# Performance work log

Hardware: AMD Instinct MI355X
Metric: run time of the kernel (lower is better)

The kernel has to match this reference:

```python
import jax, jax.numpy as jnp
import numpy as np

V, E, H, B, S = 32000, 1024, 1024, 64, 128


def setup_inputs() -> dict:
    key = jax.random.key(0)
    ks = jax.random.split(key, 16)
    s = 0.02
    return {
        "input_seq": jax.random.randint(ks[0], (B, 1), 0, V),
        "hidden": jax.random.normal(ks[1], (1, B, H), jnp.float32),
        "cell": jax.random.normal(ks[2], (1, B, H), jnp.float32),
        "encoder_outputs": jax.random.normal(ks[3], (B, S, H), jnp.float32),
        "emb": jax.random.normal(ks[4], (V, E), jnp.float32) * s,
        "Wa_w": jax.random.normal(ks[5], (H, H), jnp.float32) * s,
        "Wa_b": jnp.zeros((H,), jnp.float32),
        "Ua_w": jax.random.normal(ks[6], (H, H), jnp.float32) * s,
        "Ua_b": jnp.zeros((H,), jnp.float32),
        "Va_w": jax.random.normal(ks[7], (1, H), jnp.float32) * s,
        "Va_b": jnp.zeros((1,), jnp.float32),
        "W_ih": jax.random.normal(ks[8], (4 * H, E + H), jnp.float32) * s,
        "W_hh": jax.random.normal(ks[9], (4 * H, H), jnp.float32) * s,
        "b_ih": jnp.zeros((4 * H,), jnp.float32),
        "b_hh": jnp.zeros((4 * H,), jnp.float32),
        "out_w": jax.random.normal(ks[10], (V, H), jnp.float32) * s,
        "out_b": jnp.zeros((V,), jnp.float32),
    }


def reference(input_seq, hidden, cell, encoder_outputs, emb, Wa_w, Wa_b, Ua_w, Ua_b,
              Va_w, Va_b, W_ih, W_hh, b_ih, b_hh, out_w, out_b):
    # embedding lookup (dropout p=0 -> identity): [B,1,E]
    embedded = emb[input_seq]
    # query = last layer hidden: [B,1,H]
    query = hidden[-1][:, None, :]
    # Bahdanau additive attention
    q_proj = query @ Wa_w.T + Wa_b                       # [B,1,H]
    k_proj = encoder_outputs @ Ua_w.T + Ua_b             # [B,S,H]
    scores = jnp.tanh(q_proj + k_proj) @ Va_w.T + Va_b   # [B,S,1]
    scores = scores[..., 0][:, None, :]                  # [B,1,S]
    weights = jax.nn.softmax(scores, axis=-1)            # [B,1,S]
    context = jnp.einsum('bqs,bsh->bqh', weights, encoder_outputs)  # [B,1,H]
    # LSTM single step on concat(embedded, context)
    x = jnp.concatenate([embedded, context], axis=2)[:, 0, :]  # [B,E+H]
    h0, c0 = hidden[0], cell[0]
    gates = x @ W_ih.T + b_ih + h0 @ W_hh.T + b_hh       # [B,4H]
    i, f, g, o = jnp.split(gates, 4, axis=-1)
    c1 = jax.nn.sigmoid(f) * c0 + jax.nn.sigmoid(i) * jnp.tanh(g)
    h1 = jax.nn.sigmoid(o) * jnp.tanh(c1)
    output = h1[:, None, :]                              # [B,1,H]
    logits = output @ out_w.T + out_b                    # [B,1,V]
    return logits, h1[None], c1[None], weights
```

## Files before the change

kernel.cpp:

```cpp
#include <hip/hip_runtime.h>
#include <hip/hip_bf16.h>

using short8 = __attribute__((ext_vector_type(8))) short;
using f32x4  = __attribute__((ext_vector_type(4))) float;

__device__ inline unsigned pk2(float lo, float hi) {
    __hip_bfloat162 h = __float22bfloat162_rn(float2{lo, hi});
    return *reinterpret_cast<unsigned*>(&h);
}
__device__ inline short8 cvt8(float4 a, float4 b) {
    union { unsigned u[4]; short8 s; } r;
    r.u[0] = pk2(a.x, a.y); r.u[1] = pk2(a.z, a.w);
    r.u[2] = pk2(b.x, b.y); r.u[3] = pk2(b.z, b.w);
    return r.s;
}
__device__ inline float ftanh(float x) {
    float e = __expf(2.f * x);
    return 1.f - 2.f / (e + 1.f);
}
__device__ inline void gload16(const void* g, void* lds) {
    __builtin_amdgcn_global_load_lds(
        (const __attribute__((address_space(1))) unsigned int*)g,
        (__attribute__((address_space(3))) unsigned int*)lds, 16, 0, 0);
}
__device__ inline short f2b(float f) {
    unsigned u = __float_as_uint(f);
    return (short)((u + 0x7FFFu + ((u >> 16) & 1u)) >> 16);
}

__global__ void k_init(const int* __restrict__ idx, const float* __restrict__ emb,
                       const float* __restrict__ h0, short* __restrict__ xcat_bf,
                       float4* __restrict__ wsz) {
    int i = blockIdx.x * blockDim.x + threadIdx.x;
    if (i < 18432) {
        float4 z = {0.f, 0.f, 0.f, 0.f};
        wsz[i] = z;
    } else if (i < 34816) {
        int j = i - 18432;
        int b = j >> 8, g = j & 255;
        if (g < 128) {
            const float* p = emb + (size_t)idx[b] * 1024 + g * 8;
            *(short8*)&xcat_bf[b * 3072 + g * 8] =
                cvt8(*(const float4*)p, *(const float4*)(p + 4));
        } else {
            const float* p = h0 + (size_t)b * 1024 + (g - 128) * 8;
            *(short8*)&xcat_bf[b * 3072 + 2048 + (g - 128) * 8] =
                cvt8(*(const float4*)p, *(const float4*)(p + 4));
        }
    }
}

__global__ void k_cvt_swz(const float* __restrict__ enc, const float* __restrict__ Ua,
                          short* __restrict__ dst) {
    int i = blockIdx.x * blockDim.x + threadIdx.x;
    if (i >= 9216 * 128) return;
    int row = i >> 7, gi = i & 127;
    int seg = gi >> 3, g = gi & 7;
    const float* src = (row < 8192) ? enc + ((size_t)row << 10)
                                    : Ua + ((size_t)(row - 8192) << 10);
    const float* p = src + (seg << 6) + ((g ^ (row & 7)) << 3);
    float4 v0 = *(const float4*)p;
    float4 v1 = *(const float4*)(p + 4);
    *(short8*)&dst[(size_t)i << 3] = cvt8(v0, v1);
}

__global__ __launch_bounds__(512) void k_attn2(
    const short* __restrict__ Abf, const short* __restrict__ Bbf,
    const float* __restrict__ Uab, const float* __restrict__ Wab,
    const float* __restrict__ qp, const float* __restrict__ Va,
    float* __restrict__ scores) {
    __shared__ short As[256 * 64];
    __shared__ short Bs[128 * 64];
    const int t = threadIdx.x;
    const int l = t & 63, w = t >> 6;
    const int wm = w >> 1, wn = w & 1;
    const int lr = l & 15, lg = l >> 4;
    const int n0 = blockIdx.x * 128;
    const int r0 = blockIdx.y * 256;

    f32x4 acc[4][4];
#pragma unroll
    for (int i = 0; i < 4; ++i)
#pragma unroll
        for (int j = 0; j < 4; ++j) { f32x4 z = {0.f, 0.f, 0.f, 0.f}; acc[i][j] = z; }

    for (int seg = 0; seg < 16; ++seg) {
#pragma unroll
        for (int i = 0; i < 4; ++i) {
            int base = i * 512 + w * 64;
            int s = base + l;
            gload16(Abf + (((size_t)r0 + (s >> 3)) << 10) + (seg << 6) + ((s & 7) << 3),
                    (void*)&As[base * 8]);
            if (i < 2)
                gload16(Bbf + (((size_t)8192 + n0 + (s >> 3)) << 10) + (seg << 6) + ((s & 7) << 3),
                        (void*)&Bs[base * 8]);
        }
        __syncthreads();
#pragma unroll
        for (int kh = 0; kh < 2; ++kh) {
            short8 a[4], b[4];
#pragma unroll
            for (int i = 0; i < 4; ++i) {
                int ra = wm * 64 + i * 16 + lr;
                a[i] = *(const short8*)&As[ra * 64 + (((kh * 4 + lg) ^ (ra & 7)) << 3)];
                int rb = wn * 64 + i * 16 + lr;
                b[i] = *(const short8*)&Bs[rb * 64 + (((kh * 4 + lg) ^ (rb & 7)) << 3)];
            }
#pragma unroll
            for (int i = 0; i < 4; ++i)
#pragma unroll
                for (int j = 0; j < 4; ++j)
                    acc[i][j] = __builtin_amdgcn_mfma_f32_16x16x32_bf16(a[i], b[j], acc[i][j], 0, 0, 0);
        }
        __syncthreads();
    }

    float va[4], ub[4];
#pragma unroll
    for (int j = 0; j < 4; ++j) {
        int h = n0 + wn * 64 + j * 16 + lr;
        va[j] = Va[h];
        ub[j] = Uab[h] + Wab[h];
    }
#pragma unroll
    for (int i = 0; i < 4; ++i)
#pragma unroll
        for (int r = 0; r < 4; ++r) {
            int row = r0 + wm * 64 + i * 16 + lg * 4 + r;
            const float* qpb = qp + (size_t)(row >> 7) * 1024;
            float s = 0.f;
#pragma unroll
            for (int j = 0; j < 4; ++j) {
                int h = n0 + wn * 64 + j * 16 + lr;
                s += va[j] * ftanh(acc[i][j][r] + qpb[h] + ub[j]);
            }
            s += __shfl_xor(s, 1);
            s += __shfl_xor(s, 2);
            s += __shfl_xor(s, 4);
            s += __shfl_xor(s, 8);
            if (lr == 0) atomicAdd(scores + row, s);
        }
}

__global__ __launch_bounds__(256) void k_sgemm(
    const float* __restrict__ A, int lda,
    const float* __restrict__ B0, int ldb0,
    float* __restrict__ C, int ldc, int Kblk) {
    __shared__ short As[64 * 64];
    __shared__ short Bs[64 * 64];
    const int t = threadIdx.x;
    const int l = t & 63, w = t >> 6;
    const int wm = w >> 1, wn = w & 1;
    const int lr = l & 15, lg = l >> 4;
    const int n0 = blockIdx.x * 64;
    const int ky = blockIdx.y;

    const float* Ab = A + (size_t)ky * Kblk;
    const float* Bb = B0 + (size_t)ky * Kblk;

    f32x4 acc[2][2];
#pragma unroll
    for (int i = 0; i < 2; ++i)
#pragma unroll
        for (int j = 0; j < 2; ++j) { f32x4 z = {0.f, 0.f, 0.f, 0.f}; acc[i][j] = z; }

    for (int kt = 0; kt < Kblk; kt += 64) {
#pragma unroll
        for (int i = 0; i < 2; ++i) {
            int s = t + 256 * i, row = s >> 3, ch = s & 7;
            const float* p = Ab + (size_t)row * lda + kt + ch * 8;
            *(short8*)&As[row * 64 + ((ch ^ (row & 7)) << 3)] =
                cvt8(*(const float4*)p, *(const float4*)(p + 4));
            const float* q = Bb + (size_t)(n0 + row) * ldb0 + kt + ch * 8;
            *(short8*)&Bs[row * 64 + ((ch ^ (row & 7)) << 3)] =
                cvt8(*(const float4*)q, *(const float4*)(q + 4));
        }
        __syncthreads();
#pragma unroll
        for (int kh = 0; kh < 2; ++kh) {
            short8 a[2], b[2];
#pragma unroll
            for (int i = 0; i < 2; ++i) {
                int ra = wm * 32 + i * 16 + lr;
                a[i] = *(const short8*)&As[ra * 64 + (((kh * 4 + lg) ^ (ra & 7)) << 3)];
                int rb = wn * 32 + i * 16 + lr;
                b[i] = *(const short8*)&Bs[rb * 64 + (((kh * 4 + lg) ^ (rb & 7)) << 3)];
            }
#pragma unroll
            for (int i = 0; i < 2; ++i)
#pragma unroll
                for (int j = 0; j < 2; ++j)
                    acc[i][j] = __builtin_amdgcn_mfma_f32_16x16x32_bf16(a[i], b[j], acc[i][j], 0, 0, 0);
        }
        __syncthreads();
    }

#pragma unroll
    for (int i = 0; i < 2; ++i)
#pragma unroll
        for (int j = 0; j < 2; ++j)
#pragma unroll
            for (int r = 0; r < 4; ++r) {
                int R = wm * 32 + i * 16 + lg * 4 + r;
                int c = n0 + wn * 32 + j * 16 + lr;
                atomicAdd(&C[(size_t)R * ldc + c], acc[i][j][r]);
            }
}

__global__ __launch_bounds__(64) void k_gates_s(
    const short* __restrict__ Abf, const float* __restrict__ Wih,
    const float* __restrict__ Whh, float* __restrict__ gp) {
    const int l = threadIdx.x;
    const int lr = l & 15, lg = l >> 4;
    const int n0 = blockIdx.x * 16;
    const int ky = blockIdx.y;
    const float* Bb = (ky == 0) ? Wih : (ky == 1) ? Wih + 1024 : Whh;
    const int ldb = (ky < 2) ? 2048 : 1024;

    f32x4 acc[4];
#pragma unroll
    for (int i = 0; i < 4; ++i) { f32x4 z = {0.f, 0.f, 0.f, 0.f}; acc[i] = z; }

    const short* ap = Abf + lr * 3072 + ky * 1024 + lg * 8;
    const float* bp = Bb + (size_t)(n0 + lr) * ldb + lg * 8;

#pragma unroll 4
    for (int k0 = 0; k0 < 1024; k0 += 32) {
        float4 b0 = *(const float4*)(bp + k0);
        float4 b1 = *(const float4*)(bp + k0 + 4);
        short8 bf = cvt8(b0, b1);
        short8 a0 = *(const short8*)(ap + k0);
        short8 a1 = *(const short8*)(ap + k0 + 16 * 3072);
        short8 a2 = *(const short8*)(ap + k0 + 32 * 3072);
        short8 a3 = *(const short8*)(ap + k0 + 48 * 3072);
        acc[0] = __builtin_amdgcn_mfma_f32_16x16x32_bf16(a0, bf, acc[0], 0, 0, 0);
        acc[1] = __builtin_amdgcn_mfma_f32_16x16x32_bf16(a1, bf, acc[1], 0, 0, 0);
        acc[2] = __builtin_amdgcn_mfma_f32_16x16x32_bf16(a2, bf, acc[2], 0, 0, 0);
        acc[3] = __builtin_amdgcn_mfma_f32_16x16x32_bf16(a3, bf, acc[3], 0, 0, 0);
    }

    float* Cp = gp + (size_t)ky * 262144;
#pragma unroll
    for (int i = 0; i < 4; ++i)
#pragma unroll
        for (int r = 0; r < 4; ++r)
            Cp[(size_t)(i * 16 + lg * 4 + r) * 4096 + n0 + lr] = acc[i][r];
}

__global__ __launch_bounds__(64) void k_logits_s(
    const short* __restrict__ Abf, const float* __restrict__ B,
    const float* __restrict__ bias, float* __restrict__ C) {
    const int l = threadIdx.x;
    const int lr = l & 15, lg = l >> 4;
    const int n0 = blockIdx.x * 16;

    f32x4 acc[4];
#pragma unroll
    for (int i = 0; i < 4; ++i) { f32x4 z = {0.f, 0.f, 0.f, 0.f}; acc[i] = z; }

    const short* ap = Abf + lr * 1024 + lg * 8;
    const float* bp = B + (size_t)(n0 + lr) * 1024 + lg * 8;

#pragma unroll 4
    for (int k0 = 0; k0 < 1024; k0 += 32) {
        float4 b0 = *(const float4*)(bp + k0);
        float4 b1 = *(const float4*)(bp + k0 + 4);
        short8 bf = cvt8(b0, b1);
        short8 a0 = *(const short8*)(ap + k0);
        short8 a1 = *(const short8*)(ap + k0 + 16 * 1024);
        short8 a2 = *(const short8*)(ap + k0 + 32 * 1024);
        short8 a3 = *(const short8*)(ap + k0 + 48 * 1024);
        acc[0] = __builtin_amdgcn_mfma_f32_16x16x32_bf16(a0, bf, acc[0], 0, 0, 0);
        acc[1] = __builtin_amdgcn_mfma_f32_16x16x32_bf16(a1, bf, acc[1], 0, 0, 0);
        acc[2] = __builtin_amdgcn_mfma_f32_16x16x32_bf16(a2, bf, acc[2], 0, 0, 0);
        acc[3] = __builtin_amdgcn_mfma_f32_16x16x32_bf16(a3, bf, acc[3], 0, 0, 0);
    }

    float bv = bias[n0 + lr];
#pragma unroll
    for (int i = 0; i < 4; ++i)
#pragma unroll
        for (int r = 0; r < 4; ++r)
            C[(size_t)(i * 16 + lg * 4 + r) * 32000 + n0 + lr] = acc[i][r] + bv;
}

__global__ __launch_bounds__(256) void k_smctx(
    const float* __restrict__ scores, const float* __restrict__ enc,
    float* __restrict__ wout, short* __restrict__ xcat_bf) {
    int b = blockIdx.x;
    int t = threadIdx.x;
    __shared__ float buf[128];
    __shared__ float wsb[128];
    if (t < 128) buf[t] = scores[b * 128 + t];
    __syncthreads();
    if (t < 64) buf[t] = fmaxf(buf[t], buf[t + 64]);
    __syncthreads();
    if (t < 32) buf[t] = fmaxf(buf[t], buf[t + 32]);
    __syncthreads();
    float m;
    {
        float v = buf[t & 31];
        for (int off = 16; off > 0; off >>= 1)
            v = fmaxf(v, __shfl_xor(v, off, 32));
        m = v;
    }
    __syncthreads();
    if (t < 128) wsb[t] = __expf(scores[b * 128 + t] - m);
    __syncthreads();
    if (t < 64) buf[t] = wsb[t] + wsb[t + 64];
    __syncthreads();
    if (t < 32) buf[t] += buf[t + 32];
    __syncthreads();
    float sum;
    {
        float v = buf[t & 31];
        for (int off = 16; off > 0; off >>= 1)
            v += __shfl_xor(v, off, 32);
        sum = v;
    }
    float inv = 1.f / sum;
    __syncthreads();
    if (t < 128) {
        wsb[t] *= inv;
        wout[b * 128 + t] = wsb[t];
    }
    __syncthreads();
    float acc[4] = {0.f, 0.f, 0.f, 0.f};
    for (int s = 0; s < 128; ++s) {
        float wv = wsb[s];
        const float* row = enc + ((size_t)b * 128 + s) * 1024;
#pragma unroll
        for (int j = 0; j < 4; ++j) acc[j] += wv * row[t + 256 * j];
    }
#pragma unroll
    for (int j = 0; j < 4; ++j)
        xcat_bf[(size_t)b * 3072 + 1024 + t + 256 * j] = f2b(acc[j]);
}

__global__ void k_lstm3(const float* __restrict__ gp, const float* __restrict__ c0,
                        const float* __restrict__ b_ih, const float* __restrict__ b_hh,
                        float* __restrict__ h1, float* __restrict__ c1,
                        short* __restrict__ h1bf) {
    int idx = blockIdx.x * blockDim.x + threadIdx.x;
    int b = idx >> 10, h = idx & 1023;
    const float* g0 = gp + (size_t)b * 4096;
    float iv = b_ih[h] + b_hh[h];
    float fv = b_ih[1024 + h] + b_hh[1024 + h];
    float gv = b_ih[2048 + h] + b_hh[2048 + h];
    float ov = b_ih[3072 + h] + b_hh[3072 + h];
#pragma unroll
    for (int p = 0; p < 3; ++p) {
        const float* g = g0 + p * 262144;
        iv += g[h];
        fv += g[1024 + h];
        gv += g[2048 + h];
        ov += g[3072 + h];
    }
    float si = 1.f / (1.f + expf(-iv));
    float sf = 1.f / (1.f + expf(-fv));
    float so = 1.f / (1.f + expf(-ov));
    float tg = tanhf(gv);
    float cc = sf * c0[idx] + si * tg;
    float hh = so * tanhf(cc);
    c1[idx] = cc;
    h1[idx] = hh;
    h1bf[idx] = f2b(hh);
}

extern "C" void kernel_launch(void* const* d_in, const int* in_sizes, int n_in,
                              void* d_out, int out_size, void* d_ws, size_t ws_size,
                              hipStream_t stream) {
    const int* idx = (const int*)d_in[0];
    const float* hidden = (const float*)d_in[1];
    const float* cell = (const float*)d_in[2];
    const float* enc = (const float*)d_in[3];
    const float* emb = (const float*)d_in[4];
    const float* Wa_w = (const float*)d_in[5];
    const float* Wa_b = (const float*)d_in[6];
    const float* Ua_w = (const float*)d_in[7];
    const float* Ua_b = (const float*)d_in[8];
    const float* Va_w = (const float*)d_in[9];
    const float* W_ih = (const float*)d_in[11];
    const float* W_hh = (const float*)d_in[12];
    const float* b_ih = (const float*)d_in[13];
    const float* b_hh = (const float*)d_in[14];
    const float* out_w = (const float*)d_in[15];
    const float* out_b = (const float*)d_in[16];

    float* out = (float*)d_out;
    float* logits = out;
    float* h1 = out + 2048000;
    float* c1 = out + 2048000 + 65536;
    float* wts = out + 2048000 + 65536 + 65536;

    float* ws = (float*)d_ws;
    float* qp = ws;
    float* scores = ws + 65536;
    short* xcat_bf = (short*)(ws + 73728);
    float* gates_p = ws + 172032;
    short* h1_bf = (short*)(ws + 958464);
    short* encua_bf = (short*)(ws + 991232);

    k_init<<<136, 256, 0, stream>>>(idx, emb, hidden, xcat_bf, (float4*)ws);
    k_cvt_swz<<<4608, 256, 0, stream>>>(enc, Ua_w, encua_bf);
    k_sgemm<<<dim3(16, 8), 256, 0, stream>>>(hidden, 1024, Wa_w, 1024,
                                             qp, 1024, 128);
    k_attn2<<<dim3(8, 32), 512, 0, stream>>>(encua_bf, encua_bf, Ua_b, Wa_b,
                                             qp, Va_w, scores);
    k_smctx<<<64, 256, 0, stream>>>(scores, enc, wts, xcat_bf);
    k_gates_s<<<dim3(256, 3), 64, 0, stream>>>(xcat_bf, W_ih, W_hh, gates_p);
    k_lstm3<<<256, 256, 0, stream>>>(gates_p, cell, b_ih, b_hh, h1, c1, h1_bf);
    k_logits_s<<<2000, 64, 0, stream>>>(h1_bf, out_w, out_b, logits);
}
```

Measured before the change: 140.5 us.

## Fuse prologue kernels and overlap embedding/hidden gate GEMM with attention

Merges the init, encoder/Ua bf16 conversion and query projection into one launch, and computes qp directly without split-K atomics or zeroing. The embedding and h0 parts of the LSTM gate GEMM now run in extra blocks of the attention kernel, so only the context part remains after softmax. This cuts the launch count from eight to six. The context reduction is vectorised with float4, and the logits GEMM uses 4-wave blocks. Risks include imbalance between heterogeneous blocks in the fused kernels and lower parallelism in the 32-block gates kernel.

```diff
diff --git a/kernel.cpp b/kernel.cpp
--- a/kernel.cpp
+++ b/kernel.cpp
@@ -2,6 +2,7 @@
 #include <hip/hip_bf16.h>
 
 using short8 = __attribute__((ext_vector_type(8))) short;
+using short4v = __attribute__((ext_vector_type(4))) short;
 using f32x4  = __attribute__((ext_vector_type(4))) float;
 
 __device__ inline unsigned pk2(float lo, float hi) {
@@ -28,202 +29,8 @@
     return (short)((u + 0x7FFFu + ((u >> 16) & 1u)) >> 16);
 }
 
-__global__ void k_init(const int* __restrict__ idx, const float* __restrict__ emb,
-                       const float* __restrict__ h0, short* __restrict__ xcat_bf,
-                       float4* __restrict__ wsz) {
-    int i = blockIdx.x * blockDim.x + threadIdx.x;
-    if (i < 18432) {
-        float4 z = {0.f, 0.f, 0.f, 0.f};
-        wsz[i] = z;
-    } else if (i < 34816) {
-        int j = i - 18432;
-        int b = j >> 8, g = j & 255;
-        if (g < 128) {
-            const float* p = emb + (size_t)idx[b] * 1024 + g * 8;
-            *(short8*)&xcat_bf[b * 3072 + g * 8] =
-                cvt8(*(const float4*)p, *(const float4*)(p + 4));
-        } else {
-            const float* p = h0 + (size_t)b * 1024 + (g - 128) * 8;
-            *(short8*)&xcat_bf[b * 3072 + 2048 + (g - 128) * 8] =
-                cvt8(*(const float4*)p, *(const float4*)(p + 4));
-        }
-    }
-}
-
-__global__ void k_cvt_swz(const float* __restrict__ enc, const float* __restrict__ Ua,
-                          short* __restrict__ dst) {
-    int i = blockIdx.x * blockDim.x + threadIdx.x;
-    if (i >= 9216 * 128) return;
-    int row = i >> 7, gi = i & 127;
-    int seg = gi >> 3, g = gi & 7;
-    const float* src = (row < 8192) ? enc + ((size_t)row << 10)
-                                    : Ua + ((size_t)(row - 8192) << 10);
-    const float* p = src + (seg << 6) + ((g ^ (row & 7)) << 3);
-    float4 v0 = *(const float4*)p;
-    float4 v1 = *(const float4*)(p + 4);
-    *(short8*)&dst[(size_t)i << 3] = cvt8(v0, v1);
-}
-
-__global__ __launch_bounds__(512) void k_attn2(
-    const short* __restrict__ Abf, const short* __restrict__ Bbf,
-    const float* __restrict__ Uab, const float* __restrict__ Wab,
-    const float* __restrict__ qp, const float* __restrict__ Va,
-    float* __restrict__ scores) {
-    __shared__ short As[256 * 64];
-    __shared__ short Bs[128 * 64];
-    const int t = threadIdx.x;
-    const int l = t & 63, w = t >> 6;
-    const int wm = w >> 1, wn = w & 1;
-    const int lr = l & 15, lg = l >> 4;
-    const int n0 = blockIdx.x * 128;
-    const int r0 = blockIdx.y * 256;
-
-    f32x4 acc[4][4];
-#pragma unroll
-    for (int i = 0; i < 4; ++i)
-#pragma unroll
-        for (int j = 0; j < 4; ++j) { f32x4 z = {0.f, 0.f, 0.f, 0.f}; acc[i][j] = z; }
-
-    for (int seg = 0; seg < 16; ++seg) {
-#pragma unroll
-        for (int i = 0; i < 4; ++i) {
-            int base = i * 512 + w * 64;
-            int s = base + l;
-            gload16(Abf + (((size_t)r0 + (s >> 3)) << 10) + (seg << 6) + ((s & 7) << 3),
-                    (void*)&As[base * 8]);
-            if (i < 2)
-                gload16(Bbf + (((size_t)8192 + n0 + (s >> 3)) << 10) + (seg << 6) + ((s & 7) << 3),
-                        (void*)&Bs[base * 8]);
-        }
-        __syncthreads();
-#pragma unroll
-        for (int kh = 0; kh < 2; ++kh) {
-            short8 a[4], b[4];
-#pragma unroll
-            for (int i = 0; i < 4; ++i) {
-                int ra = wm * 64 + i * 16 + lr;
-                a[i] = *(const short8*)&As[ra * 64 + (((kh * 4 + lg) ^ (ra & 7)) << 3)];
-                int rb = wn * 64 + i * 16 + lr;
-                b[i] = *(const short8*)&Bs[rb * 64 + (((kh * 4 + lg) ^ (rb & 7)) << 3)];
-            }
-#pragma unroll
-            for (int i = 0; i < 4; ++i)
-#pragma unroll
-                for (int j = 0; j < 4; ++j)
-                    acc[i][j] = __builtin_amdgcn_mfma_f32_16x16x32_bf16(a[i], b[j], acc[i][j], 0, 0, 0);
-        }
-        __syncthreads();
-    }
-
-    float va[4], ub[4];
-#pragma unroll
-    for (int j = 0; j < 4; ++j) {
-        int h = n0 + wn * 64 + j * 16 + lr;
-        va[j] = Va[h];
-        ub[j] = Uab[h] + Wab[h];
-    }
-#pragma unroll
-    for (int i = 0; i < 4; ++i)
-#pragma unroll
-        for (int r = 0; r < 4; ++r) {
-            int row = r0 + wm * 64 + i * 16 + lg * 4 + r;
-            const float* qpb = qp + (size_t)(row >> 7) * 1024;
-            float s = 0.f;
-#pragma unroll
-            for (int j = 0; j < 4; ++j) {
-                int h = n0 + wn * 64 + j * 16 + lr;
-                s += va[j] * ftanh(acc[i][j][r] + qpb[h] + ub[j]);
-            }
-            s += __shfl_xor(s, 1);
-            s += __shfl_xor(s, 2);
-            s += __shfl_xor(s, 4);
-            s += __shfl_xor(s, 8);
-            if (lr == 0) atomicAdd(scores + row, s);
-        }
-}
-
-__global__ __launch_bounds__(256) void k_sgemm(
-    const float* __restrict__ A, int lda,
-    const float* __restrict__ B0, int ldb0,
-    float* __restrict__ C, int ldc, int Kblk) {
-    __shared__ short As[64 * 64];
-    __shared__ short Bs[64 * 64];
-    const int t = threadIdx.x;
-    const int l = t & 63, w = t >> 6;
-    const int wm = w >> 1, wn = w & 1;
-    const int lr = l & 15, lg = l >> 4;
-    const int n0 = blockIdx.x * 64;
-    const int ky = blockIdx.y;
-
-    const float* Ab = A + (size_t)ky * Kblk;
-    const float* Bb = B0 + (size_t)ky * Kblk;
-
-    f32x4 acc[2][2];
-#pragma unroll
-    for (int i = 0; i < 2; ++i)
-#pragma unroll
-        for (int j = 0; j < 2; ++j) { f32x4 z = {0.f, 0.f, 0.f, 0.f}; acc[i][j] = z; }
-
-    for (int kt = 0; kt < Kblk; kt += 64) {
-#pragma unroll
-        for (int i = 0; i < 2; ++i) {
-            int s = t + 256 * i, row = s >> 3, ch = s & 7;
-            const float* p = Ab + (size_t)row * lda + kt + ch * 8;
-            *(short8*)&As[row * 64 + ((ch ^ (row & 7)) << 3)] =
-                cvt8(*(const float4*)p, *(const float4*)(p + 4));
-            const float* q = Bb + (size_t)(n0 + row) * ldb0 + kt + ch * 8;
-            *(short8*)&Bs[row * 64 + ((ch ^ (row & 7)) << 3)] =
-                cvt8(*(const float4*)q, *(const float4*)(q + 4));
-        }
-        __syncthreads();
-#pragma unroll
-        for (int kh = 0; kh < 2; ++kh) {
-            short8 a[2], b[2];
-#pragma unroll
-            for (int i = 0; i < 2; ++i) {
-                int ra = wm * 32 + i * 16 + lr;
-                a[i] = *(const short8*)&As[ra * 64 + (((kh * 4 + lg) ^ (ra & 7)) << 3)];
-                int rb = wn * 32 + i * 16 + lr;
-                b[i] = *(const short8*)&Bs[rb * 64 + (((kh * 4 + lg) ^ (rb & 7)) << 3)];
-            }
-#pragma unroll
-            for (int i = 0; i < 2; ++i)
-#pragma unroll
-                for (int j = 0; j < 2; ++j)
-                    acc[i][j] = __builtin_amdgcn_mfma_f32_16x16x32_bf16(a[i], b[j], acc[i][j], 0, 0, 0);
-        }
-        __syncthreads();
-    }
-
-#pragma unroll
-    for (int i = 0; i < 2; ++i)
-#pragma unroll
-        for (int j = 0; j < 2; ++j)
-#pragma unroll
-            for (int r = 0; r < 4; ++r) {
-                int R = wm * 32 + i * 16 + lg * 4 + r;
-                int c = n0 + wn * 32 + j * 16 + lr;
-                atomicAdd(&C[(size_t)R * ldc + c], acc[i][j][r]);
-            }
-}
-
-__global__ __launch_bounds__(64) void k_gates_s(
-    const short* __restrict__ Abf, const float* __restrict__ Wih,
-    const float* __restrict__ Whh, float* __restrict__ gp) {
-    const int l = threadIdx.x;
-    const int lr = l & 15, lg = l >> 4;
-    const int n0 = blockIdx.x * 16;
-    const int ky = blockIdx.y;
-    const float* Bb = (ky == 0) ? Wih : (ky == 1) ? Wih + 1024 : Whh;
-    const int ldb = (ky < 2) ? 2048 : 1024;
-
-    f32x4 acc[4];
-#pragma unroll
-    for (int i = 0; i < 4; ++i) { f32x4 z = {0.f, 0.f, 0.f, 0.f}; acc[i] = z; }
-
-    const short* ap = Abf + lr * 3072 + ky * 1024 + lg * 8;
-    const float* bp = Bb + (size_t)(n0 + lr) * ldb + lg * 8;
-
+__device__ inline void xcat_pass(const short* __restrict__ ap,
+                                 const float* __restrict__ bp, f32x4 (&acc)[4]) {
 #pragma unroll 4
     for (int k0 = 0; k0 < 1024; k0 += 32) {
         float4 b0 = *(const float4*)(bp + k0);
@@ -238,50 +45,166 @@
         acc[2] = __builtin_amdgcn_mfma_f32_16x16x32_bf16(a2, bf, acc[2], 0, 0, 0);
         acc[3] = __builtin_amdgcn_mfma_f32_16x16x32_bf16(a3, bf, acc[3], 0, 0, 0);
     }
-
-    float* Cp = gp + (size_t)ky * 262144;
-#pragma unroll
-    for (int i = 0; i < 4; ++i)
-#pragma unroll
-        for (int r = 0; r < 4; ++r)
-            Cp[(size_t)(i * 16 + lg * 4 + r) * 4096 + n0 + lr] = acc[i][r];
-}
-
-__global__ __launch_bounds__(64) void k_logits_s(
-    const short* __restrict__ Abf, const float* __restrict__ B,
-    const float* __restrict__ bias, float* __restrict__ C) {
-    const int l = threadIdx.x;
+}
+
+__global__ __launch_bounds__(512) void k_fused1(
+    const float* __restrict__ enc, const float* __restrict__ Ua,
+    short* __restrict__ encua_bf,
+    const float* __restrict__ hidden, const float* __restrict__ Wa,
+    float* __restrict__ qp,
+    const int* __restrict__ idx, const float* __restrict__ emb,
+    short* __restrict__ xcat_bf, float4* __restrict__ scores4) {
+    const int bid = blockIdx.x, t = threadIdx.x;
+    if (bid < 2304) {
+        int i = bid * 512 + t;
+        int row = i >> 7, gi = i & 127;
+        int seg = gi >> 3, g = gi & 7;
+        const float* src = (row < 8192) ? enc + ((size_t)row << 10)
+                                        : Ua + ((size_t)(row - 8192) << 10);
+        const float* p = src + (seg << 6) + ((g ^ (row & 7)) << 3);
+        *(short8*)&encua_bf[(size_t)i << 3] =
+            cvt8(*(const float4*)p, *(const float4*)(p + 4));
+    } else if (bid < 2312) {
+        const int l = t & 63, wv = t >> 6;
+        const int lr = l & 15, lg = l >> 4;
+        const int n0 = (bid - 2304) * 128 + wv * 16;
+        f32x4 acc[4];
+#pragma unroll
+        for (int i = 0; i < 4; ++i) { f32x4 z = {0.f, 0.f, 0.f, 0.f}; acc[i] = z; }
+        const float* ap = hidden + lr * 1024 + lg * 8;
+        const float* bp = Wa + (size_t)(n0 + lr) * 1024 + lg * 8;
+#pragma unroll 4
+        for (int k0 = 0; k0 < 1024; k0 += 32) {
+            short8 bf = cvt8(*(const float4*)(bp + k0), *(const float4*)(bp + k0 + 4));
+            short8 a0 = cvt8(*(const float4*)(ap + k0), *(const float4*)(ap + k0 + 4));
+            short8 a1 = cvt8(*(const float4*)(ap + k0 + 16384), *(const float4*)(ap + k0 + 16388));
+            short8 a2 = cvt8(*(const float4*)(ap + k0 + 32768), *(const float4*)(ap + k0 + 32772));
+            short8 a3 = cvt8(*(const float4*)(ap + k0 + 49152), *(const float4*)(ap + k0 + 49156));
+            acc[0] = __builtin_amdgcn_mfma_f32_16x16x32_bf16(a0, bf, acc[0], 0, 0, 0);
+            acc[1] = __builtin_amdgcn_mfma_f32_16x16x32_bf16(a1, bf, acc[1], 0, 0, 0);
+            acc[2] = __builtin_amdgcn_mfma_f32_16x16x32_bf16(a2, bf, acc[2], 0, 0, 0);
+            acc[3] = __builtin_amdgcn_mfma_f32_16x16x32_bf16(a3, bf, acc[3], 0, 0, 0);
+        }
+#pragma unroll
+        for (int i = 0; i < 4; ++i)
+#pragma unroll
+            for (int r = 0; r < 4; ++r)
+                qp[(size_t)(i * 16 + lg * 4 + r) * 1024 + n0 + lr] = acc[i][r];
+    } else {
+        int j = (bid - 2312) * 512 + t;
+        if (j < 16384) {
+            int b = j >> 8, g = j & 255;
+            if (g < 128) {
+                const float* p = emb + (size_t)idx[b] * 1024 + g * 8;
+                *(short8*)&xcat_bf[b * 3072 + g * 8] =
+                    cvt8(*(const float4*)p, *(const float4*)(p + 4));
+            } else {
+                const float* p = hidden + (size_t)b * 1024 + (g - 128) * 8;
+                *(short8*)&xcat_bf[b * 3072 + 2048 + (g - 128) * 8] =
+                    cvt8(*(const float4*)p, *(const float4*)(p + 4));
+            }
+        } else {
+            float4 z = {0.f, 0.f, 0.f, 0.f};
+            scores4[j - 16384] = z;
+        }
+    }
+}
+
+__global__ __launch_bounds__(512) void k_attn_gates(
+    const short* __restrict__ encua_bf,
+    const float* __restrict__ Uab, const float* __restrict__ Wab,
+    const float* __restrict__ qp, const float* __restrict__ Va,
+    float* __restrict__ scores,
+    const short* __restrict__ xcat_bf, const float* __restrict__ Wih,
+    const float* __restrict__ Whh, float* __restrict__ gp0) {
+    __shared__ short As[256 * 64];
+    __shared__ short Bs[128 * 64];
+    const int bid = blockIdx.x, t = threadIdx.x;
+    const int l = t & 63, w = t >> 6;
     const int lr = l & 15, lg = l >> 4;
-    const int n0 = blockIdx.x * 16;
-
-    f32x4 acc[4];
-#pragma unroll
-    for (int i = 0; i < 4; ++i) { f32x4 z = {0.f, 0.f, 0.f, 0.f}; acc[i] = z; }
-
-    const short* ap = Abf + lr * 1024 + lg * 8;
-    const float* bp = B + (size_t)(n0 + lr) * 1024 + lg * 8;
-
-#pragma unroll 4
-    for (int k0 = 0; k0 < 1024; k0 += 32) {
-        float4 b0 = *(const float4*)(bp + k0);
-        float4 b1 = *(const float4*)(bp + k0 + 4);
-        short8 bf = cvt8(b0, b1);
-        short8 a0 = *(const short8*)(ap + k0);
-        short8 a1 = *(const short8*)(ap + k0 + 16 * 1024);
-        short8 a2 = *(const short8*)(ap + k0 + 32 * 1024);
-        short8 a3 = *(const short8*)(ap + k0 + 48 * 1024);
-        acc[0] = __builtin_amdgcn_mfma_f32_16x16x32_bf16(a0, bf, acc[0], 0, 0, 0);
-        acc[1] = __builtin_amdgcn_mfma_f32_16x16x32_bf16(a1, bf, acc[1], 0, 0, 0);
-        acc[2] = __builtin_amdgcn_mfma_f32_16x16x32_bf16(a2, bf, acc[2], 0, 0, 0);
-        acc[3] = __builtin_amdgcn_mfma_f32_16x16x32_bf16(a3, bf, acc[3], 0, 0, 0);
-    }
-
-    float bv = bias[n0 + lr];
-#pragma unroll
-    for (int i = 0; i < 4; ++i)
-#pragma unroll
-        for (int r = 0; r < 4; ++r)
-            C[(size_t)(i * 16 + lg * 4 + r) * 32000 + n0 + lr] = acc[i][r] + bv;
+
+    if (bid < 256) {
+        const int wm = w >> 1, wn = w & 1;
+        const int n0 = (bid & 7) * 128;
+        const int r0 = (bid >> 3) * 256;
+
+        f32x4 acc[4][4];
+#pragma unroll
+        for (int i = 0; i < 4; ++i)
+#pragma unroll
+            for (int j = 0; j < 4; ++j) { f32x4 z = {0.f, 0.f, 0.f, 0.f}; acc[i][j] = z; }
+
+        for (int seg = 0; seg < 16; ++seg) {
+#pragma unroll
+            for (int i = 0; i < 4; ++i) {
+                int base = i * 512 + w * 64;
+                int s = base + l;
+                gload16(encua_bf + (((size_t)r0 + (s >> 3)) << 10) + (seg << 6) + ((s & 7) << 3),
+                        (void*)&As[base * 8]);
+                if (i < 2)
+                    gload16(encua_bf + (((size_t)8192 + n0 + (s >> 3)) << 10) + (seg << 6) + ((s & 7) << 3),
+                            (void*)&Bs[base * 8]);
+            }
+            __syncthreads();
+#pragma unroll
+            for (int kh = 0; kh < 2; ++kh) {
+                short8 a[4], b[4];
+#pragma unroll
+                for (int i = 0; i < 4; ++i) {
+                    int ra = wm * 64 + i * 16 + lr;
+                    a[i] = *(const short8*)&As[ra * 64 + (((kh * 4 + lg) ^ (ra & 7)) << 3)];
+                    int rb = wn * 64 + i * 16 + lr;
+                    b[i] = *(const short8*)&Bs[rb * 64 + (((kh * 4 + lg) ^ (rb & 7)) << 3)];
+                }
+#pragma unroll
+                for (int i = 0; i < 4; ++i)
+#pragma unroll
+                    for (int j = 0; j < 4; ++j)
+                        acc[i][j] = __builtin_amdgcn_mfma_f32_16x16x32_bf16(a[i], b[j], acc[i][j], 0, 0, 0);
+            }
+            __syncthreads();
+        }
+
+        float va[4], ub[4];
+#pragma unroll
+        for (int j = 0; j < 4; ++j) {
+            int h = n0 + wn * 64 + j * 16 + lr;
+            va[j] = Va[h];
+            ub[j] = Uab[h] + Wab[h];
+        }
+#pragma unroll
+        for (int i = 0; i < 4; ++i)
+#pragma unroll
+            for (int r = 0; r < 4; ++r) {
+                int row = r0 + wm * 64 + i * 16 + lg * 4 + r;
+                const float* qpb = qp + (size_t)(row >> 7) * 1024;
+                float s = 0.f;
+#pragma unroll
+                for (int j = 0; j < 4; ++j) {
+                    int h = n0 + wn * 64 + j * 16 + lr;
+                    s += va[j] * ftanh(acc[i][j][r] + qpb[h] + ub[j]);
+                }
+                s += __shfl_xor(s, 1);
+                s += __shfl_xor(s, 2);
+                s += __shfl_xor(s, 4);
+                s += __shfl_xor(s, 8);
+                if (lr == 0) atomicAdd(scores + row, s);
+            }
+    } else {
+        const int n0 = (bid - 256) * 128 + w * 16;
+        f32x4 acc[4];
+#pragma unroll
+        for (int i = 0; i < 4; ++i) { f32x4 z = {0.f, 0.f, 0.f, 0.f}; acc[i] = z; }
+        xcat_pass(xcat_bf + lr * 3072 + lg * 8,
+                  Wih + (size_t)(n0 + lr) * 2048 + lg * 8, acc);
+        xcat_pass(xcat_bf + lr * 3072 + 2048 + lg * 8,
+                  Whh + (size_t)(n0 + lr) * 1024 + lg * 8, acc);
+#pragma unroll
+        for (int i = 0; i < 4; ++i)
+#pragma unroll
+            for (int r = 0; r < 4; ++r)
+                gp0[(size_t)(i * 16 + lg * 4 + r) * 4096 + n0 + lr] = acc[i][r];
+    }
 }
 
 __global__ __launch_bounds__(256) void k_smctx(
@@ -325,19 +248,39 @@
         wout[b * 128 + t] = wsb[t];
     }
     __syncthreads();
-    float acc[4] = {0.f, 0.f, 0.f, 0.f};
+    float4 acc = {0.f, 0.f, 0.f, 0.f};
+    const float* base = enc + (size_t)b * 131072 + t * 4;
     for (int s = 0; s < 128; ++s) {
         float wv = wsb[s];
-        const float* row = enc + ((size_t)b * 128 + s) * 1024;
-#pragma unroll
-        for (int j = 0; j < 4; ++j) acc[j] += wv * row[t + 256 * j];
-    }
-#pragma unroll
-    for (int j = 0; j < 4; ++j)
-        xcat_bf[(size_t)b * 3072 + 1024 + t + 256 * j] = f2b(acc[j]);
-}
-
-__global__ void k_lstm3(const float* __restrict__ gp, const float* __restrict__ c0,
+        float4 v = *(const float4*)(base + s * 1024);
+        acc.x += wv * v.x; acc.y += wv * v.y;
+        acc.z += wv * v.z; acc.w += wv * v.w;
+    }
+    short4v o;
+    o[0] = f2b(acc.x); o[1] = f2b(acc.y); o[2] = f2b(acc.z); o[3] = f2b(acc.w);
+    *(short4v*)&xcat_bf[(size_t)b * 3072 + 1024 + t * 4] = o;
+}
+
+__global__ __launch_bounds__(512) void k_gates2(
+    const short* __restrict__ xcat_bf, const float* __restrict__ Wih,
+    float* __restrict__ gp1) {
+    const int t = threadIdx.x;
+    const int l = t & 63, w = t >> 6;
+    const int lr = l & 15, lg = l >> 4;
+    const int n0 = blockIdx.x * 128 + w * 16;
+    f32x4 acc[4];
+#pragma unroll
+    for (int i = 0; i < 4; ++i) { f32x4 z = {0.f, 0.f, 0.f, 0.f}; acc[i] = z; }
+    xcat_pass(xcat_bf + lr * 3072 + 1024 + lg * 8,
+              Wih + (size_t)(n0 + lr) * 2048 + 1024 + lg * 8, acc);
+#pragma unroll
+    for (int i = 0; i < 4; ++i)
+#pragma unroll
+        for (int r = 0; r < 4; ++r)
+            gp1[(size_t)(i * 16 + lg * 4 + r) * 4096 + n0 + lr] = acc[i][r];
+}
+
+__global__ void k_lstm2(const float* __restrict__ gp, const float* __restrict__ c0,
                         const float* __restrict__ b_ih, const float* __restrict__ b_hh,
                         float* __restrict__ h1, float* __restrict__ c1,
                         short* __restrict__ h1bf) {
@@ -349,7 +292,7 @@
     float gv = b_ih[2048 + h] + b_hh[2048 + h];
     float ov = b_ih[3072 + h] + b_hh[3072 + h];
 #pragma unroll
-    for (int p = 0; p < 3; ++p) {
+    for (int p = 0; p < 2; ++p) {
         const float* g = g0 + p * 262144;
         iv += g[h];
         fv += g[1024 + h];
@@ -365,6 +308,44 @@
     c1[idx] = cc;
     h1[idx] = hh;
     h1bf[idx] = f2b(hh);
+}
+
+__global__ __launch_bounds__(256) void k_vgemm(
+    const short* __restrict__ Abf, const float* __restrict__ B,
+    const float* __restrict__ bias, float* __restrict__ C) {
+    const int t = threadIdx.x;
+    const int l = t & 63, w = t >> 6;
+    const int lr = l & 15, lg = l >> 4;
+    const int n0 = blockIdx.x * 64 + w * 16;
+
+    f32x4 acc[4];
+#pragma unroll
+    for (int i = 0; i < 4; ++i) { f32x4 z = {0.f, 0.f, 0.f, 0.f}; acc[i] = z; }
+
+    const float* bp = B + (size_t)(n0 + lr) * 1024 + lg * 8;
+    const short* ap = Abf + lr * 1024 + lg * 8;
+
+#pragma unroll 4
+    for (int k0 = 0; k0 < 1024; k0 += 32) {
+        float4 b0 = *(const float4*)(bp + k0);
+        float4 b1 = *(const float4*)(bp + k0 + 4);
+        short8 a0 = *(const short8*)(ap + k0);
+        short8 a1 = *(const short8*)(ap + k0 + 16 * 1024);
+        short8 a2 = *(const short8*)(ap + k0 + 32 * 1024);
+        short8 a3 = *(const short8*)(ap + k0 + 48 * 1024);
+        short8 bf = cvt8(b0, b1);
+        acc[0] = __builtin_amdgcn_mfma_f32_16x16x32_bf16(a0, bf, acc[0], 0, 0, 0);
+        acc[1] = __builtin_amdgcn_mfma_f32_16x16x32_bf16(a1, bf, acc[1], 0, 0, 0);
+        acc[2] = __builtin_amdgcn_mfma_f32_16x16x32_bf16(a2, bf, acc[2], 0, 0, 0);
+        acc[3] = __builtin_amdgcn_mfma_f32_16x16x32_bf16(a3, bf, acc[3], 0, 0, 0);
+    }
+
+    float bv = bias[n0 + lr];
+#pragma unroll
+    for (int i = 0; i < 4; ++i)
+#pragma unroll
+        for (int r = 0; r < 4; ++r)
+            C[(size_t)(i * 16 + lg * 4 + r) * 32000 + n0 + lr] = acc[i][r] + bv;
 }
 
 extern "C" void kernel_launch(void* const* d_in, const int* in_sizes, int n_in,
@@ -398,17 +379,15 @@
     float* scores = ws + 65536;
     short* xcat_bf = (short*)(ws + 73728);
     float* gates_p = ws + 172032;
-    short* h1_bf = (short*)(ws + 958464);
-    short* encua_bf = (short*)(ws + 991232);
-
-    k_init<<<136, 256, 0, stream>>>(idx, emb, hidden, xcat_bf, (float4*)ws);
-    k_cvt_swz<<<4608, 256, 0, stream>>>(enc, Ua_w, encua_bf);
-    k_sgemm<<<dim3(16, 8), 256, 0, stream>>>(hidden, 1024, Wa_w, 1024,
-                                             qp, 1024, 128);
-    k_attn2<<<dim3(8, 32), 512, 0, stream>>>(encua_bf, encua_bf, Ua_b, Wa_b,
-                                             qp, Va_w, scores);
+    short* h1_bf = (short*)(ws + 696320);
+    short* encua_bf = (short*)(ws + 729088);
+
+    k_fused1<<<2348, 512, 0, stream>>>(enc, Ua_w, encua_bf, hidden, Wa_w, qp,
+                                       idx, emb, xcat_bf, (float4*)scores);
+    k_attn_gates<<<288, 512, 0, stream>>>(encua_bf, Ua_b, Wa_b, qp, Va_w, scores,
+                                          xcat_bf, W_ih, W_hh, gates_p);
     k_smctx<<<64, 256, 0, stream>>>(scores, enc, wts, xcat_bf);
-    k_gates_s<<<dim3(256, 3), 64, 0, stream>>>(xcat_bf, W_ih, W_hh, gates_p);
-    k_lstm3<<<256, 256, 0, stream>>>(gates_p, cell, b_ih, b_hh, h1, c1, h1_bf);
-    k_logits_s<<<2000, 64, 0, stream>>>(h1_bf, out_w, out_b, logits);
-}
+    k_gates2<<<32, 512, 0, stream>>>(xcat_bf, W_ih, gates_p + 262144);
+    k_lstm2<<<256, 256, 0, stream>>>(gates_p, cell, b_ih, b_hh, h1, c1, h1_bf);
+    k_vgemm<<<500, 256, 0, stream>>>(h1_bf, out_w, out_b, logits);
+}
```

Measured after the change: 299.3 us. 2.13x slower.
